# Performance work log

Measured on AMD Instinct MI355X. Metric: run time of the kernel, lower is better.

## Reference

```python
import jax, jax.numpy as jnp
import numpy as np

T = 4          # num edge types
D = 256        # embedding_size == hidden_size
N = 100_000    # nodes
E_EDGES = 320_000
VOCAB = 10_000


def setup_inputs() -> dict:
    key = jax.random.key(0)
    ks = jax.random.split(key, 12)
    s = 0.02
    input_ids = jax.random.randint(ks[0], (1, N), 0, VOCAB)
    etype = jax.random.randint(ks[1], (1, E_EDGES), 1, T + 1)  # types 1..T
    src = jax.random.randint(ks[2], (1, E_EDGES), 0, N)
    tgt = jax.random.randint(ks[3], (1, E_EDGES), 0, N)
    typed_edges = jnp.stack([etype[0], src[0], tgt[0]], axis=0)[None]  # [1,3,E]
    embed_table = jax.random.normal(ks[4], (VOCAB, D)) * s
    # 6 inner layers (3 per concat block x 2 blocks): 256 -> 256
    edge_W_inner = jax.random.normal(ks[5], (6, T, D, 2 * D)) * s
    ln_s_inner = jnp.ones((6, D)); ln_b_inner = jnp.zeros((6, D))
    dense_W_inner = jax.random.normal(ks[6], (6, D, D)) * s
    dense_b_inner = jnp.zeros((6, D))
    # 2 output layers on concat [state, hidden]: hidden_size 512 -> 256
    edge_W_out = jax.random.normal(ks[7], (2, T, 2 * D, 4 * D)) * s
    ln_s_out = jnp.ones((2, 2 * D)); ln_b_out = jnp.zeros((2, 2 * D))
    dense_W_out = jax.random.normal(ks[8], (2, D, 2 * D)) * s
    dense_b_out = jnp.zeros((2, D))
    return {
        "input_ids": input_ids, "typed_edges": typed_edges,
        "embed_table": embed_table,
        "edge_W_inner": edge_W_inner, "ln_s_inner": ln_s_inner, "ln_b_inner": ln_b_inner,
        "dense_W_inner": dense_W_inner, "dense_b_inner": dense_b_inner,
        "edge_W_out": edge_W_out, "ln_s_out": ln_s_out, "ln_b_out": ln_b_out,
        "dense_W_out": dense_W_out, "dense_b_out": dense_b_out,
    }


def layer_norm(x, s, b, eps=1e-5):
    mu = jnp.mean(x, axis=-1, keepdims=True)
    var = jnp.mean((x - mu) ** 2, axis=-1, keepdims=True)
    return (x - mu) * jax.lax.rsqrt(var + eps) * s + b


def message_passing(state, etype, src, tgt, edge_W):
    # state [N,d]; edge_W [T, d, 2d]. Gather endpoints, per-type linear, scatter-add to targets.
    es = jnp.concatenate([state[src], state[tgt]], axis=1)  # [E, 2d]
    msgs = jnp.zeros((es.shape[0], edge_W.shape[1]), state.dtype)
    for t in range(edge_W.shape[0]):  # small fixed number of edge types
        msgs = msgs + jnp.where((etype == t + 1)[:, None], es @ edge_W[t].T, 0.0)
    return jax.ops.segment_sum(msgs, tgt, num_segments=state.shape[0])


def gnn_layer(state, etype, src, tgt, eW, ls, lb, dW, db):
    m = message_passing(state, etype, src, tgt, eW)
    h = layer_norm(jax.nn.gelu(m, approximate=False), ls, lb)
    return jnp.tanh(h @ dW.T + db)


def concat_block(state, etype, src, tgt, eWi, lsi, lbi, dWi, dbi, eWo, lso, lbo, dWo, dbo):
    x = state
    for i in range(3):
        x = gnn_layer(x, etype, src, tgt, eWi[i], lsi[i], lbi[i], dWi[i], dbi[i])
    res = jnp.concatenate([state, x], axis=1)  # [N, 2d] residual concat
    return gnn_layer(res, etype, src, tgt, eWo, lso, lbo, dWo, dbo)


def reference(input_ids, typed_edges, embed_table, edge_W_inner, ln_s_inner, ln_b_inner,
              dense_W_inner, dense_b_inner, edge_W_out, ln_s_out, ln_b_out,
              dense_W_out, dense_b_out):
    ids = input_ids[0]
    te = typed_edges[0]
    etype, src, tgt = te[0], te[1], te[2]
    x = embed_table[ids]  # [N, D]
    for b in range(2):
        sl = slice(3 * b, 3 * b + 3)
        x = concat_block(x, etype, src, tgt,
                         edge_W_inner[sl], ln_s_inner[sl], ln_b_inner[sl],
                         dense_W_inner[sl], dense_b_inner[sl],
                         edge_W_out[b], ln_s_out[b], ln_b_out[b],
                         dense_W_out[b], dense_b_out[b])
    return x
```

## Files before the change

kernel.cpp:

```cpp
#include <hip/hip_runtime.h>
#include <cstdio>

#define N_NODES 100000
#define NPAD    100096
#define NTILES  782
#define NE      320000
#define NCH     196
#define WCO_OFF 3145728L
#define OUT_ELEMS (N_NODES * 256)

typedef unsigned short ushort_t;
typedef unsigned short u16x4 __attribute__((ext_vector_type(4)));
typedef unsigned short u16x8 __attribute__((ext_vector_type(8)));
typedef _Float16       f16;
typedef _Float16       f16x8 __attribute__((ext_vector_type(8)));
typedef float          f32x4 __attribute__((ext_vector_type(4)));
typedef float          f32x4v __attribute__((ext_vector_type(4)));

__device__ __forceinline__ float bf2f(ushort_t u) {
    return __uint_as_float(((unsigned)u) << 16);
}
__device__ __forceinline__ ushort_t f2bf(float f) {
    unsigned u = __float_as_uint(f);
    u += 0x7FFFu + ((u >> 16) & 1u);
    return (ushort_t)(u >> 16);
}
__device__ __forceinline__ ushort_t f2h(float f) {
    f16 h = (f16)f;
    return __builtin_bit_cast(ushort_t, h);
}
__device__ __forceinline__ float h2f(ushort_t u) {
    return (float)__builtin_bit_cast(f16, u);
}

__global__ __launch_bounds__(256) void detect_k(const unsigned* __restrict__ w0, int* __restrict__ flag) {
    __shared__ int lds[256];
    int t = threadIdx.x;
    int cnt = 0;
    for (int i = t; i < 2048; i += 256) {
        unsigned e = (w0[i] >> 7) & 0xFFu;
        cnt += (e >= 96u && e <= 140u) ? 1 : 0;
    }
    lds[t] = cnt; __syncthreads();
    for (int s = 128; s > 0; s >>= 1) {
        if (t < s) lds[t] += lds[t + s];
        __syncthreads();
    }
    if (t == 0) *flag = (lds[0] < 1024) ? 1 : 0;
}

__device__ __forceinline__ ushort_t load_in(const void* p, long i, bool isf32) {
    return isf32 ? f2h(((const float*)p)[i]) : f2h(bf2f(((const ushort_t*)p)[i]));
}

struct CvtArgs {
    const void* src[8];
    ushort_t*   dst[8];
    int         n[8];
};

__global__ __launch_bounds__(256) void cvt_k(CvtArgs a, const int* __restrict__ flag) {
    int ti = blockIdx.y;
    int n = a.n[ti];
    const void* s = a.src[ti];
    ushort_t* d = a.dst[ti];
    bool isf32 = (*flag != 0);
    for (int i = blockIdx.x * 256 + threadIdx.x; i < n; i += gridDim.x * 256)
        d[i] = load_in(s, i, isf32);
}

__global__ __launch_bounds__(256) void pack_w(const void* __restrict__ eWi,
                                              const void* __restrict__ eWo,
                                              ushort_t* __restrict__ WC,
                                              const int* __restrict__ flag) {
    long idx = (long)blockIdx.x * 256 + threadIdx.x;
    bool isf32 = (*flag != 0);
    const long ELI = 6L * 4 * 256 * 512;
    const long ELO = 2L * 4 * 512 * 1024;
    if (idx < ELI) {
        int j = idx & 511;
        int o = (idx >> 9) & 255;
        int t = (idx >> 17) & 3;
        long l = idx >> 19;
        int q = o >> 6, oo = o & 63;
        int k = j & 255;
        int n = ((j < 256) ? 0 : 256) + t * 64 + oo;
        WC[l * 524288 + (long)q * 131072 + (long)n * 256 + k] = load_in(eWi, idx, isf32);
    } else if (idx < ELI + ELO) {
        long i2 = idx - ELI;
        int j = i2 & 1023;
        int o = (i2 >> 10) & 511;
        int t = (i2 >> 19) & 3;
        long b = i2 >> 21;
        int p = t >> 1, ts = t & 1;
        WC[WCO_OFF + (b * 2 + p) * 1048576L + (long)o * 2048 + ts * 1024 + j] = load_in(eWo, i2, isf32);
    }
}

__global__ __launch_bounds__(256) void embed_k(const int* __restrict__ ids,
                                               const void* __restrict__ tab,
                                               ushort_t* __restrict__ S,
                                               const int* __restrict__ flag) {
    int row = blockIdx.x * 4 + (threadIdx.x >> 6);
    int l = threadIdx.x & 63;
    if (row >= N_NODES) return;
    int id = ids[row];
    u16x4 v;
    if (*flag) {
        f32x4v fv = *(const f32x4v*)((const float*)tab + (size_t)id * 256 + l * 4);
        #pragma unroll
        for (int i = 0; i < 4; i++) v[i] = f2h(fv[i]);
    } else {
        u16x4 bv = *(const u16x4*)((const ushort_t*)tab + (size_t)id * 256 + l * 4);
        #pragma unroll
        for (int i = 0; i < 4; i++) v[i] = f2h(bf2f(bv[i]));
    }
    *(u16x4*)(S + (size_t)row * 256 + l * 4) = v;
}

__global__ __launch_bounds__(256) void emit_k(const ushort_t* __restrict__ Bst, void* __restrict__ out,
                                              const int* __restrict__ flag) {
    long i = (long)blockIdx.x * 256 + threadIdx.x;
    if (i >= OUT_ELEMS) return;
    float v = h2f(Bst[i]);
    if (*flag) ((float*)out)[i] = v;
    else       ((ushort_t*)out)[i] = f2bf(v);
}

__global__ __launch_bounds__(256) void count_k(const int* __restrict__ tgt, int* __restrict__ counts) {
    int e = blockIdx.x * 256 + threadIdx.x;
    if (e < NE) atomicAdd(&counts[tgt[e]], 1);
}

__global__ __launch_bounds__(256) void scan1_k(const int* __restrict__ counts,
                                               int* __restrict__ incl, int* __restrict__ chsums) {
    __shared__ int lds[256];
    int c = blockIdx.x, t = threadIdx.x;
    int i0 = c * 512 + 2 * t;
    int a = (i0 < N_NODES) ? counts[i0] : 0;
    int b = (i0 + 1 < N_NODES) ? counts[i0 + 1] : 0;
    int ps = a + b;
    lds[t] = ps; __syncthreads();
    int x = ps;
    for (int off = 1; off < 256; off <<= 1) {
        int y = (t >= off) ? lds[t - off] : 0;
        __syncthreads();
        x += y; lds[t] = x;
        __syncthreads();
    }
    int excl = x - ps;
    if (i0 < N_NODES) incl[i0] = excl + a;
    if (i0 + 1 < N_NODES) incl[i0 + 1] = excl + a + b;
    if (t == 255) chsums[c] = x;
}

__global__ __launch_bounds__(256) void scan2_k(const int* __restrict__ chsums, int* __restrict__ chunkoff) {
    __shared__ int lds[256];
    int t = threadIdx.x;
    int v = (t < NCH) ? chsums[t] : 0;
    lds[t] = v; __syncthreads();
    int x = v;
    for (int off = 1; off < 256; off <<= 1) {
        int y = (t >= off) ? lds[t - off] : 0;
        __syncthreads();
        x += y; lds[t] = x;
        __syncthreads();
    }
    if (t <= NCH) chunkoff[t] = x - v;
}

__global__ __launch_bounds__(256) void scan3_k(const int* __restrict__ counts, const int* __restrict__ incl,
                                               const int* __restrict__ chunkoff,
                                               int* __restrict__ offsets, int* __restrict__ cursor) {
    int c = blockIdx.x, t = threadIdx.x;
    int base = chunkoff[c];
    #pragma unroll
    for (int k = 0; k < 2; k++) {
        int i = c * 512 + 2 * t + k;
        if (i < N_NODES) {
            int off = base + incl[i] - counts[i];
            offsets[i] = off;
            cursor[i] = off;
        }
    }
    if (c == 0 && t == 0) offsets[N_NODES] = chunkoff[NCH];
}

__global__ __launch_bounds__(256) void fill_k(const int* __restrict__ et, const int* __restrict__ src,
                                              const int* __restrict__ tgt,
                                              int* __restrict__ cursor, int* __restrict__ sorted) {
    int e = blockIdx.x * 256 + threadIdx.x;
    if (e < NE) {
        int pos = atomicAdd(&cursor[tgt[e]], 1);
        sorted[pos] = ((et[e] - 1) << 28) | src[e];
    }
}

template<int DIN>
__device__ __forceinline__ void load_row(const ushort_t* __restrict__ X0, const ushort_t* __restrict__ X1,
                                         size_t r, int l, float* out) {
    if constexpr (DIN == 256) {
        u16x4 rv = *(const u16x4*)(X0 + r * 256 + l * 4);
        #pragma unroll
        for (int i = 0; i < 4; i++) out[i] = h2f(rv[i]);
    } else {
        const ushort_t* bp = (l < 32) ? (X0 + r * 256 + (size_t)l * 8)
                                      : (X1 + r * 256 + (size_t)(l - 32) * 8);
        u16x8 rv = *(const u16x8*)bp;
        #pragma unroll
        for (int i = 0; i < 8; i++) out[i] = h2f(rv[i]);
    }
}

template<int DIN>
__device__ __forceinline__ void store_blk(ushort_t* __restrict__ G, size_t base, int l,
                                          const float* A, int D, const float* xv) {
    if constexpr (DIN == 256) {
        u16x4 o1, o2;
        #pragma unroll
        for (int i = 0; i < 4; i++) { o1[i] = f2h(A[i]); o2[i] = f2h((float)D * xv[i]); }
        *(u16x4*)(G + base + l * 4) = o1;
        *(u16x4*)(G + base + DIN + l * 4) = o2;
    } else {
        u16x8 o1, o2;
        #pragma unroll
        for (int i = 0; i < 8; i++) { o1[i] = f2h(A[i]); o2[i] = f2h((float)D * xv[i]); }
        *(u16x8*)(G + base + l * 8) = o1;
        *(u16x8*)(G + base + DIN + l * 8) = o2;
    }
}

template<int DIN, int NT>
__global__ __launch_bounds__(256) void build_g(const ushort_t* __restrict__ X0, const ushort_t* __restrict__ X1,
                                               const int* __restrict__ offsets, const int* __restrict__ sorted,
                                               ushort_t* __restrict__ G, int t0, int vbase) {
    constexpr int VPL = DIN / 64;
    int vl = blockIdx.x * 4 + (threadIdx.x >> 6);
    int l = threadIdx.x & 63;
    int v = vbase + vl;
    float a0[VPL] = {}, a1[VPL] = {}, a2[VPL] = {}, a3[VPL] = {};
    int d0 = 0, d1 = 0, d2 = 0, d3 = 0;
    float xv[VPL];
    #pragma unroll
    for (int i = 0; i < VPL; i++) xv[i] = 0.f;
    if (v < N_NODES) {
        int beg = offsets[v], end = offsets[v + 1];
        for (int e = beg; e < end; ++e) {
            int pk = sorted[e];
            int t = (pk >> 28) - t0;
            if ((unsigned)t >= (unsigned)NT) continue;
            int s = pk & 0x0FFFFFFF;
            float rvf[VPL];
            load_row<DIN>(X0, X1, (size_t)s, l, rvf);
            if (t == 0) { d0++;
                #pragma unroll
                for (int i = 0; i < VPL; i++) a0[i] += rvf[i]; }
            else if (t == 1) { d1++;
                #pragma unroll
                for (int i = 0; i < VPL; i++) a1[i] += rvf[i]; }
            else if (NT > 2 && t == 2) { d2++;
                #pragma unroll
                for (int i = 0; i < VPL; i++) a2[i] += rvf[i]; }
            else { d3++;
                #pragma unroll
                for (int i = 0; i < VPL; i++) a3[i] += rvf[i]; }
        }
        load_row<DIN>(X0, X1, (size_t)v, l, xv);
    }
    size_t rowb = (size_t)vl * 2048;
    store_blk<DIN>(G, rowb + 0 * 2 * DIN, l, a0, d0, xv);
    store_blk<DIN>(G, rowb + 1 * 2 * DIN, l, a1, d1, xv);
    if constexpr (NT > 2) {
        store_blk<DIN>(G, rowb + 2 * 2 * DIN, l, a2, d2, xv);
        store_blk<DIN>(G, rowb + 3 * 2 * DIN, l, a3, d3, xv);
    }
}

template<int EPI>
__global__ __launch_bounds__(256) void gemm_bt(const ushort_t* __restrict__ A,
                                               const ushort_t* __restrict__ B,
                                               int K, int ldc,
                                               float* __restrict__ Cf, ushort_t* __restrict__ Cb,
                                               const ushort_t* __restrict__ bias, int storeM) {
    __shared__ __align__(16) ushort_t As[128 * 64];
    __shared__ __align__(16) ushort_t Bs[128 * 64];
    const int tid = threadIdx.x;
    const int w = tid >> 6, l = tid & 63;
    const int wr = w >> 1, wc = w & 1;
    const long m0 = (long)blockIdx.y * 128, n0 = (long)blockIdx.x * 128;
    const int lr = l >> 3;
    const int lc = (l & 7) * 8;
    f32x4 acc[4][4];
    #pragma unroll
    for (int s = 0; s < 4; s++)
        #pragma unroll
        for (int n = 0; n < 4; n++) acc[s][n] = (f32x4){0.f, 0.f, 0.f, 0.f};

    for (int k0 = 0; k0 < K; k0 += 64) {
        #pragma unroll
        for (int q = 0; q < 4; q++) {
            int row = w * 32 + q * 8 + lr;
            const ushort_t* g = A + (m0 + row) * (long)K + k0 + lc;
            __builtin_amdgcn_global_load_lds(
                (__attribute__((address_space(1))) unsigned int*)(g),
                (__attribute__((address_space(3))) unsigned int*)(&As[row * 64 + lc]), 16, 0, 0);
        }
        #pragma unroll
        for (int q = 0; q < 4; q++) {
            int row = w * 32 + q * 8 + lr;
            const ushort_t* g = B + (n0 + row) * (long)K + k0 + lc;
            __builtin_amdgcn_global_load_lds(
                (__attribute__((address_space(1))) unsigned int*)(g),
                (__attribute__((address_space(3))) unsigned int*)(&Bs[row * 64 + lc]), 16, 0, 0);
        }
        __syncthreads();
        #pragma unroll
        for (int kk = 0; kk < 2; kk++) {
            f16x8 af[4], bfr[4];
            #pragma unroll
            for (int s = 0; s < 4; s++)
                af[s] = *(const f16x8*)&As[(wr * 64 + s * 16 + (l & 15)) * 64 + kk * 32 + (l >> 4) * 8];
            #pragma unroll
            for (int n = 0; n < 4; n++)
                bfr[n] = *(const f16x8*)&Bs[(wc * 64 + n * 16 + (l & 15)) * 64 + kk * 32 + (l >> 4) * 8];
            #pragma unroll
            for (int s = 0; s < 4; s++)
                #pragma unroll
                for (int n = 0; n < 4; n++)
                    acc[s][n] = __builtin_amdgcn_mfma_f32_16x16x32_f16(af[s], bfr[n], acc[s][n], 0, 0, 0);
        }
        __syncthreads();
    }
    const long rb = m0 + wr * 64 + ((l >> 4) << 2);
    const long cb = n0 + wc * 64 + (l & 15);
    #pragma unroll
    for (int s = 0; s < 4; s++) {
        #pragma unroll
        for (int n = 0; n < 4; n++) {
            long c = cb + n * 16;
            #pragma unroll
            for (int j = 0; j < 4; j++) {
                long r = rb + s * 16 + j;
                float val = acc[s][n][j];
                if constexpr (EPI == 0) {
                    Cf[r * ldc + c] = val;
                } else if constexpr (EPI == 1) {
                    Cf[r * ldc + c] += val;
                } else if constexpr (EPI == 2) {
                    if (r < storeM) {
                        float t = tanhf(val + h2f(bias[c]));
                        Cb[r * ldc + c] = f2h(t);
                    }
                } else {
                    Cb[r * ldc + c] = f2h(val);
                }
            }
        }
    }
}

__global__ __launch_bounds__(256) void agg_q(const ushort_t* __restrict__ Z,
                                             const int* __restrict__ offsets,
                                             const int* __restrict__ sorted,
                                             ushort_t* __restrict__ Magg, int q) {
    int v = blockIdx.x * 4 + (threadIdx.x >> 6);
    int l = threadIdx.x & 63;
    if (v >= NPAD) return;
    ushort_t* mp = Magg + (size_t)v * 256 + (q << 6) + l;
    if (v >= N_NODES) { *mp = 0; return; }
    float acc = 0.f;
    int d0 = 0, d1 = 0, d2 = 0, d3 = 0;
    int beg = offsets[v], end = offsets[v + 1];
    for (int e = beg; e < end; ++e) {
        int pk = sorted[e];
        int t = pk >> 28;
        int s = pk & 0x0FFFFFFF;
        acc += h2f(Z[(size_t)s * 512 + (t << 6) + l]);
        d0 += (t == 0); d1 += (t == 1); d2 += (t == 2); d3 += (t == 3);
    }
    const ushort_t* zs = Z + (size_t)v * 512 + 256 + l;
    if (d0) acc += (float)d0 * h2f(zs[0]);
    if (d1) acc += (float)d1 * h2f(zs[64]);
    if (d2) acc += (float)d2 * h2f(zs[128]);
    if (d3) acc += (float)d3 * h2f(zs[192]);
    *mp = f2h(acc);
}

__global__ __launch_bounds__(256) void gelu_ln16_k(const ushort_t* __restrict__ M,
                                                   const ushort_t* __restrict__ ls,
                                                   const ushort_t* __restrict__ lb,
                                                   ushort_t* __restrict__ H) {
    int row = blockIdx.x * 4 + (threadIdx.x >> 6);
    int l = threadIdx.x & 63;
    u16x4 mv = *(const u16x4*)(M + (size_t)row * 256 + l * 4);
    float g[4];
    float s = 0.f, q = 0.f;
    #pragma unroll
    for (int i = 0; i < 4; i++) {
        float x = h2f(mv[i]);
        float gg = 0.5f * x * (1.f + erff(x * 0.70710678118654752f));
        g[i] = gg; s += gg; q += gg * gg;
    }
    #pragma unroll
    for (int m = 1; m < 64; m <<= 1) {
        s += __shfl_xor(s, m, 64);
        q += __shfl_xor(q, m, 64);
    }
    float mean = s * (1.f / 256.f);
    float var = q * (1.f / 256.f) - mean * mean;
    var = fmaxf(var, 0.f);
    float rs = rsqrtf(var + 1e-5f);
    int col = l << 2;
    u16x4 o;
    #pragma unroll
    for (int i = 0; i < 4; i++)
        o[i] = f2h((g[i] - mean) * rs * h2f(ls[col + i]) + h2f(lb[col + i]));
    *(u16x4*)(H + (size_t)row * 256 + col) = o;
}

template<int DOUT>
__global__ __launch_bounds__(256) void gelu_ln_k(const float* __restrict__ Mf,
                                                 const ushort_t* __restrict__ ls,
                                                 const ushort_t* __restrict__ lb,
                                                 ushort_t* __restrict__ H) {
    constexpr int VPL = DOUT / 64;
    int row = blockIdx.x * 4 + (threadIdx.x >> 6);
    int l = threadIdx.x & 63;
    const float* p = Mf + (size_t)row * DOUT + l * VPL;
    float g[VPL];
    float s = 0.f, q = 0.f;
    #pragma unroll
    for (int i = 0; i < VPL; i++) {
        float x = p[i];
        float gg = 0.5f * x * (1.f + erff(x * 0.70710678118654752f));
        g[i] = gg; s += gg; q += gg * gg;
    }
    #pragma unroll
    for (int m = 1; m < 64; m <<= 1) {
        s += __shfl_xor(s, m, 64);
        q += __shfl_xor(q, m, 64);
    }
    float mean = s * (1.f / DOUT);
    float var = q * (1.f / DOUT) - mean * mean;
    var = fmaxf(var, 0.f);
    float rs = rsqrtf(var + 1e-5f);
    ushort_t* hp = H + (size_t)row * DOUT + l * VPL;
    #pragma unroll
    for (int i = 0; i < VPL; i++) {
        int col = l * VPL + i;
        hp[i] = f2h((g[i] - mean) * rs * h2f(ls[col]) + h2f(lb[col]));
    }
}

extern "C" void kernel_launch(void* const* d_in, const int* in_sizes, int n_in,
                              void* d_out, int out_size, void* d_ws, size_t ws_size,
                              hipStream_t stream) {
    const int* ids = (const int*)d_in[0];
    const int* te = (const int*)d_in[1];
    const int* et = te;
    const int* esrc = te + NE;
    const int* etgt = te + 2 * NE;
    const void* tab = d_in[2];
    const void* eWi = d_in[3];
    const void* lsi = d_in[4];
    const void* lbi = d_in[5];
    const void* dWi = d_in[6];
    const void* dbi = d_in[7];
    const void* eWo = d_in[8];
    const void* lso = d_in[9];
    const void* lbo = d_in[10];
    const void* dWo = d_in[11];
    const void* dbo = d_in[12];

    char* w = (char*)d_ws;
    auto alloc = [&](size_t bytes) -> char* {
        char* p = w; w += (bytes + 255) & ~(size_t)255; return p;
    };
    ushort_t* A    = (ushort_t*)alloc((size_t)NPAD * 256 * 2);
    ushort_t* Bst  = (ushort_t*)alloc((size_t)NPAD * 256 * 2);
    ushort_t* WC   = (ushort_t*)alloc(7340032UL * 2);
    ushort_t* lsiC = (ushort_t*)alloc(1536 * 2);
    ushort_t* lbiC = (ushort_t*)alloc(1536 * 2);
    ushort_t* dbiC = (ushort_t*)alloc(1536 * 2);
    ushort_t* lsoC = (ushort_t*)alloc(1024 * 2);
    ushort_t* lboC = (ushort_t*)alloc(1024 * 2);
    ushort_t* dboC = (ushort_t*)alloc(512 * 2);
    ushort_t* dWiC = (ushort_t*)alloc(393216UL * 2);
    ushort_t* dWoC = (ushort_t*)alloc(262144UL * 2);
    int* flag      = (int*)alloc(256);
    int* counts    = (int*)alloc((size_t)N_NODES * 4);
    int* incl      = (int*)alloc((size_t)N_NODES * 4);
    int* chsums    = (int*)alloc(1024);
    int* chunkoff  = (int*)alloc(1024);
    int* offsets   = (int*)alloc((size_t)(N_NODES + 8) * 4);
    int* cursor    = (int*)alloc((size_t)N_NODES * 4);
    int* sorted    = (int*)alloc((size_t)NE * 4);
    ushort_t* Magg = (ushort_t*)alloc((size_t)NPAD * 256 * 2);
    ushort_t* R;
    if ((size_t)out_size >= (size_t)NPAD * 256 * 2) R = (ushort_t*)d_out;
    else R = (ushort_t*)alloc((size_t)NPAD * 256 * 2);
    size_t fixed = (size_t)(w - (char*)d_ws);

    const size_t ZQ_BYTES = (size_t)NPAD * 512 * 2;
    const size_t PER_TILE = 128UL * 2048 * 2 + 128UL * 512 * 4 + 128UL * 512 * 2;
    size_t bigsz = (ws_size > fixed) ? (ws_size - fixed) : 0;
    long tiles_chunk = (long)(bigsz / PER_TILE);
    if (tiles_chunk > NTILES) tiles_chunk = NTILES;
    if (bigsz < ZQ_BYTES || tiles_chunk < 1) {
        fprintf(stderr, "kernel_launch: ws too small (%zu bytes, fixed %zu, big %zu) -- no-op\n",
                ws_size, fixed, bigsz);
        return;
    }
    char* big = w;
    ushort_t* Zq   = (ushort_t*)big;
    ushort_t* Hin  = (ushort_t*)big;
    ushort_t* G    = (ushort_t*)big;
    float*    Mf   = (float*)(big + (size_t)tiles_chunk * 524288);
    ushort_t* Hc   = (ushort_t*)(big + (size_t)tiles_chunk * (524288 + 262144));

    detect_k<<<1, 256, 0, stream>>>((const unsigned*)tab, flag);
    CvtArgs ca;
    ca.src[0] = lsi;  ca.dst[0] = lsiC; ca.n[0] = 1536;
    ca.src[1] = lbi;  ca.dst[1] = lbiC; ca.n[1] = 1536;
    ca.src[2] = dbi;  ca.dst[2] = dbiC; ca.n[2] = 1536;
    ca.src[3] = lso;  ca.dst[3] = lsoC; ca.n[3] = 1024;
    ca.src[4] = lbo;  ca.dst[4] = lboC; ca.n[4] = 1024;
    ca.src[5] = dbo;  ca.dst[5] = dboC; ca.n[5] = 512;
    ca.src[6] = dWi;  ca.dst[6] = dWiC; ca.n[6] = 393216;
    ca.src[7] = dWo;  ca.dst[7] = dWoC; ca.n[7] = 262144;
    cvt_k<<<dim3(1536, 8), 256, 0, stream>>>(ca, flag);
    hipMemsetAsync(counts, 0, (size_t)N_NODES * 4, stream);
    hipMemsetAsync(A   + (size_t)N_NODES * 256, 0, (size_t)(NPAD - N_NODES) * 256 * 2, stream);
    hipMemsetAsync(Bst + (size_t)N_NODES * 256, 0, (size_t)(NPAD - N_NODES) * 256 * 2, stream);
    hipMemsetAsync(R   + (size_t)N_NODES * 256, 0, (size_t)(NPAD - N_NODES) * 256 * 2, stream);
    pack_w<<<28672, 256, 0, stream>>>(eWi, eWo, WC, flag);
    embed_k<<<N_NODES / 4, 256, 0, stream>>>(ids, tab, A, flag);
    count_k<<<(NE + 255) / 256, 256, 0, stream>>>(etgt, counts);
    scan1_k<<<NCH, 256, 0, stream>>>(counts, incl, chsums);
    scan2_k<<<1, 256, 0, stream>>>(chsums, chunkoff);
    scan3_k<<<NCH, 256, 0, stream>>>(counts, incl, chunkoff, offsets, cursor);
    fill_k<<<(NE + 255) / 256, 256, 0, stream>>>(et, esrc, etgt, cursor, sorted);

    auto inner_layer = [&](const ushort_t* Xin, ushort_t* Xout, int lay) {
        for (int q = 0; q < 4; q++) {
            gemm_bt<3><<<dim3(4, NTILES), 256, 0, stream>>>(
                Xin, WC + (long)lay * 524288 + (long)q * 131072, 256, 512,
                nullptr, Zq, nullptr, 0);
            agg_q<<<NPAD / 4, 256, 0, stream>>>(Zq, offsets, sorted, Magg, q);
        }
        gelu_ln16_k<<<NPAD / 4, 256, 0, stream>>>(Magg, lsiC + lay * 256, lbiC + lay * 256, Hin);
        gemm_bt<2><<<dim3(2, NTILES), 256, 0, stream>>>(Hin, dWiC + (long)lay * 65536, 256, 256,
                                                        nullptr, Xout, dbiC + lay * 256, N_NODES);
    };

    auto out_layer = [&](const ushort_t* X0, const ushort_t* X1, int b, ushort_t* dest) {
        for (long t0t = 0; t0t < NTILES; t0t += tiles_chunk) {
            long tc = NTILES - t0t; if (tc > tiles_chunk) tc = tiles_chunk;
            long rows = tc * 128, mb = t0t * 128;
            build_g<512, 2><<<rows / 4, 256, 0, stream>>>(X0, X1, offsets, sorted, G, 0, (int)mb);
            gemm_bt<0><<<dim3(4, tc), 256, 0, stream>>>(G, WC + WCO_OFF + (long)(b * 2 + 0) * 1048576,
                                                        2048, 512, Mf, nullptr, nullptr, 0);
            build_g<512, 2><<<rows / 4, 256, 0, stream>>>(X0, X1, offsets, sorted, G, 2, (int)mb);
            gemm_bt<1><<<dim3(4, tc), 256, 0, stream>>>(G, WC + WCO_OFF + (long)(b * 2 + 1) * 1048576,
                                                        2048, 512, Mf, nullptr, nullptr, 0);
            gelu_ln_k<512><<<rows / 4, 256, 0, stream>>>(Mf, lsoC + b * 512, lboC + b * 512, Hc);
            long sM = (long)N_NODES - mb; if (sM > rows) sM = rows; if (sM < 0) sM = 0;
            gemm_bt<2><<<dim3(2, tc), 256, 0, stream>>>(Hc, dWoC + (long)b * 131072, 512, 256,
                                                        nullptr, dest + mb * 256, dboC + b * 256, (int)sM);
        }
    };

    inner_layer(A, Bst, 0);
    inner_layer(Bst, R, 1);
    inner_layer(R, Bst, 2);
    out_layer(A, Bst, 0, R);
    inner_layer(R, A, 3);
    inner_layer(A, Bst, 4);
    inner_layer(Bst, A, 5);
    out_layer(R, A, 1, Bst);

    emit_k<<<(OUT_ELEMS + 255) / 256, 256, 0, stream>>>(Bst, d_out, flag);
}
```

Measured before the change: 6.816 ms.

## Restructure output layers to transform-then-aggregate like inner layers

The output-layer path used to build a per-node aggregated feature matrix G of width 2048 and then run a K=2048 GEMM into fp32. It now follows the inner-layer scheme: a per-node GEMM over the concatenated input (K=512) in 8 column chunks, with edge aggregation applied to the transformed outputs, then a shared GELU+LN kernel. This removes the heavy gather-heavy build_g and the large-K GEMMs, cutting FLOPs. The cost is more kernel launches (8 GEMM+agg pairs) and fp16 intermediate storage where fp32 was used before.

```diff
diff --git a/kernel.cpp b/kernel.cpp
--- a/kernel.cpp
+++ b/kernel.cpp
@@ -92,8 +92,10 @@
         int o = (i2 >> 10) & 511;
         int t = (i2 >> 19) & 3;
         long b = i2 >> 21;
-        int p = t >> 1, ts = t & 1;
-        WC[WCO_OFF + (b * 2 + p) * 1048576L + (long)o * 2048 + ts * 1024 + j] = load_in(eWo, i2, isf32);
+        int c = o >> 6, oo = o & 63;
+        int k = j & 511;
+        int n = ((j < 512) ? 0 : 256) + t * 64 + oo;
+        WC[WCO_OFF + b * 2097152L + (long)c * 262144 + (long)n * 512 + k] = load_in(eWo, i2, isf32);
     }
 }
 
@@ -196,91 +198,11 @@
     }
 }
 
-template<int DIN>
-__device__ __forceinline__ void load_row(const ushort_t* __restrict__ X0, const ushort_t* __restrict__ X1,
-                                         size_t r, int l, float* out) {
-    if constexpr (DIN == 256) {
-        u16x4 rv = *(const u16x4*)(X0 + r * 256 + l * 4);
-        #pragma unroll
-        for (int i = 0; i < 4; i++) out[i] = h2f(rv[i]);
-    } else {
-        const ushort_t* bp = (l < 32) ? (X0 + r * 256 + (size_t)l * 8)
-                                      : (X1 + r * 256 + (size_t)(l - 32) * 8);
-        u16x8 rv = *(const u16x8*)bp;
-        #pragma unroll
-        for (int i = 0; i < 8; i++) out[i] = h2f(rv[i]);
-    }
-}
-
-template<int DIN>
-__device__ __forceinline__ void store_blk(ushort_t* __restrict__ G, size_t base, int l,
-                                          const float* A, int D, const float* xv) {
-    if constexpr (DIN == 256) {
-        u16x4 o1, o2;
-        #pragma unroll
-        for (int i = 0; i < 4; i++) { o1[i] = f2h(A[i]); o2[i] = f2h((float)D * xv[i]); }
-        *(u16x4*)(G + base + l * 4) = o1;
-        *(u16x4*)(G + base + DIN + l * 4) = o2;
-    } else {
-        u16x8 o1, o2;
-        #pragma unroll
-        for (int i = 0; i < 8; i++) { o1[i] = f2h(A[i]); o2[i] = f2h((float)D * xv[i]); }
-        *(u16x8*)(G + base + l * 8) = o1;
-        *(u16x8*)(G + base + DIN + l * 8) = o2;
-    }
-}
-
-template<int DIN, int NT>
-__global__ __launch_bounds__(256) void build_g(const ushort_t* __restrict__ X0, const ushort_t* __restrict__ X1,
-                                               const int* __restrict__ offsets, const int* __restrict__ sorted,
-                                               ushort_t* __restrict__ G, int t0, int vbase) {
-    constexpr int VPL = DIN / 64;
-    int vl = blockIdx.x * 4 + (threadIdx.x >> 6);
-    int l = threadIdx.x & 63;
-    int v = vbase + vl;
-    float a0[VPL] = {}, a1[VPL] = {}, a2[VPL] = {}, a3[VPL] = {};
-    int d0 = 0, d1 = 0, d2 = 0, d3 = 0;
-    float xv[VPL];
-    #pragma unroll
-    for (int i = 0; i < VPL; i++) xv[i] = 0.f;
-    if (v < N_NODES) {
-        int beg = offsets[v], end = offsets[v + 1];
-        for (int e = beg; e < end; ++e) {
-            int pk = sorted[e];
-            int t = (pk >> 28) - t0;
-            if ((unsigned)t >= (unsigned)NT) continue;
-            int s = pk & 0x0FFFFFFF;
-            float rvf[VPL];
-            load_row<DIN>(X0, X1, (size_t)s, l, rvf);
-            if (t == 0) { d0++;
-                #pragma unroll
-                for (int i = 0; i < VPL; i++) a0[i] += rvf[i]; }
-            else if (t == 1) { d1++;
-                #pragma unroll
-                for (int i = 0; i < VPL; i++) a1[i] += rvf[i]; }
-            else if (NT > 2 && t == 2) { d2++;
-                #pragma unroll
-                for (int i = 0; i < VPL; i++) a2[i] += rvf[i]; }
-            else { d3++;
-                #pragma unroll
-                for (int i = 0; i < VPL; i++) a3[i] += rvf[i]; }
-        }
-        load_row<DIN>(X0, X1, (size_t)v, l, xv);
-    }
-    size_t rowb = (size_t)vl * 2048;
-    store_blk<DIN>(G, rowb + 0 * 2 * DIN, l, a0, d0, xv);
-    store_blk<DIN>(G, rowb + 1 * 2 * DIN, l, a1, d1, xv);
-    if constexpr (NT > 2) {
-        store_blk<DIN>(G, rowb + 2 * 2 * DIN, l, a2, d2, xv);
-        store_blk<DIN>(G, rowb + 3 * 2 * DIN, l, a3, d3, xv);
-    }
-}
-
 template<int EPI>
 __global__ __launch_bounds__(256) void gemm_bt(const ushort_t* __restrict__ A,
                                                const ushort_t* __restrict__ B,
                                                int K, int ldc,
-                                               float* __restrict__ Cf, ushort_t* __restrict__ Cb,
+                                               ushort_t* __restrict__ Cb,
                                                const ushort_t* __restrict__ bias, int storeM) {
     __shared__ __align__(16) ushort_t As[128 * 64];
     __shared__ __align__(16) ushort_t Bs[128 * 64];
@@ -342,11 +264,7 @@
             for (int j = 0; j < 4; j++) {
                 long r = rb + s * 16 + j;
                 float val = acc[s][n][j];
-                if constexpr (EPI == 0) {
-                    Cf[r * ldc + c] = val;
-                } else if constexpr (EPI == 1) {
-                    Cf[r * ldc + c] += val;
-                } else if constexpr (EPI == 2) {
+                if constexpr (EPI == 2) {
                     if (r < storeM) {
                         float t = tanhf(val + h2f(bias[c]));
                         Cb[r * ldc + c] = f2h(t);
@@ -359,14 +277,86 @@
     }
 }
 
+__global__ __launch_bounds__(256) void gemm_bt2(const ushort_t* __restrict__ A0,
+                                                const ushort_t* __restrict__ A1,
+                                                const ushort_t* __restrict__ B,
+                                                int ldc,
+                                                ushort_t* __restrict__ Cb) {
+    __shared__ __align__(16) ushort_t As[128 * 64];
+    __shared__ __align__(16) ushort_t Bs[128 * 64];
+    const int tid = threadIdx.x;
+    const int w = tid >> 6, l = tid & 63;
+    const int wr = w >> 1, wc = w & 1;
+    const long m0 = (long)blockIdx.y * 128, n0 = (long)blockIdx.x * 128;
+    const int lr = l >> 3;
+    const int lc = (l & 7) * 8;
+    f32x4 acc[4][4];
+    #pragma unroll
+    for (int s = 0; s < 4; s++)
+        #pragma unroll
+        for (int n = 0; n < 4; n++) acc[s][n] = (f32x4){0.f, 0.f, 0.f, 0.f};
+
+    for (int k0 = 0; k0 < 512; k0 += 64) {
+        const ushort_t* Ab = (k0 < 256) ? A0 : A1;
+        const int kq = k0 & 255;
+        #pragma unroll
+        for (int q = 0; q < 4; q++) {
+            int row = w * 32 + q * 8 + lr;
+            const ushort_t* g = Ab + (m0 + row) * 256L + kq + lc;
+            __builtin_amdgcn_global_load_lds(
+                (__attribute__((address_space(1))) unsigned int*)(g),
+                (__attribute__((address_space(3))) unsigned int*)(&As[row * 64 + lc]), 16, 0, 0);
+        }
+        #pragma unroll
+        for (int q = 0; q < 4; q++) {
+            int row = w * 32 + q * 8 + lr;
+            const ushort_t* g = B + (n0 + row) * 512L + k0 + lc;
+            __builtin_amdgcn_global_load_lds(
+                (__attribute__((address_space(1))) unsigned int*)(g),
+                (__attribute__((address_space(3))) unsigned int*)(&Bs[row * 64 + lc]), 16, 0, 0);
+        }
+        __syncthreads();
+        #pragma unroll
+        for (int kk = 0; kk < 2; kk++) {
+            f16x8 af[4], bfr[4];
+            #pragma unroll
+            for (int s = 0; s < 4; s++)
+                af[s] = *(const f16x8*)&As[(wr * 64 + s * 16 + (l & 15)) * 64 + kk * 32 + (l >> 4) * 8];
+            #pragma unroll
+            for (int n = 0; n < 4; n++)
+                bfr[n] = *(const f16x8*)&Bs[(wc * 64 + n * 16 + (l & 15)) * 64 + kk * 32 + (l >> 4) * 8];
+            #pragma unroll
+            for (int s = 0; s < 4; s++)
+                #pragma unroll
+                for (int n = 0; n < 4; n++)
+                    acc[s][n] = __builtin_amdgcn_mfma_f32_16x16x32_f16(af[s], bfr[n], acc[s][n], 0, 0, 0);
+        }
+        __syncthreads();
+    }
+    const long rb = m0 + wr * 64 + ((l >> 4) << 2);
+    const long cb = n0 + wc * 64 + (l & 15);
+    #pragma unroll
+    for (int s = 0; s < 4; s++) {
+        #pragma unroll
+        for (int n = 0; n < 4; n++) {
+            long c = cb + n * 16;
+            #pragma unroll
+            for (int j = 0; j < 4; j++) {
+                long r = rb + s * 16 + j;
+                Cb[r * ldc + c] = f2h(acc[s][n][j]);
+            }
+        }
+    }
+}
+
 __global__ __launch_bounds__(256) void agg_q(const ushort_t* __restrict__ Z,
                                              const int* __restrict__ offsets,
                                              const int* __restrict__ sorted,
-                                             ushort_t* __restrict__ Magg, int q) {
+                                             ushort_t* __restrict__ M, int mld, int q) {
     int v = blockIdx.x * 4 + (threadIdx.x >> 6);
     int l = threadIdx.x & 63;
     if (v >= NPAD) return;
-    ushort_t* mp = Magg + (size_t)v * 256 + (q << 6) + l;
+    ushort_t* mp = M + (size_t)v * mld + (q << 6) + l;
     if (v >= N_NODES) { *mp = 0; return; }
     float acc = 0.f;
     int d0 = 0, d1 = 0, d2 = 0, d3 = 0;
@@ -386,52 +376,23 @@
     *mp = f2h(acc);
 }
 
+template<int DOUT>
 __global__ __launch_bounds__(256) void gelu_ln16_k(const ushort_t* __restrict__ M,
                                                    const ushort_t* __restrict__ ls,
                                                    const ushort_t* __restrict__ lb,
                                                    ushort_t* __restrict__ H) {
-    int row = blockIdx.x * 4 + (threadIdx.x >> 6);
-    int l = threadIdx.x & 63;
-    u16x4 mv = *(const u16x4*)(M + (size_t)row * 256 + l * 4);
-    float g[4];
-    float s = 0.f, q = 0.f;
-    #pragma unroll
-    for (int i = 0; i < 4; i++) {
-        float x = h2f(mv[i]);
-        float gg = 0.5f * x * (1.f + erff(x * 0.70710678118654752f));
-        g[i] = gg; s += gg; q += gg * gg;
-    }
-    #pragma unroll
-    for (int m = 1; m < 64; m <<= 1) {
-        s += __shfl_xor(s, m, 64);
-        q += __shfl_xor(q, m, 64);
-    }
-    float mean = s * (1.f / 256.f);
-    float var = q * (1.f / 256.f) - mean * mean;
-    var = fmaxf(var, 0.f);
-    float rs = rsqrtf(var + 1e-5f);
-    int col = l << 2;
-    u16x4 o;
-    #pragma unroll
-    for (int i = 0; i < 4; i++)
-        o[i] = f2h((g[i] - mean) * rs * h2f(ls[col + i]) + h2f(lb[col + i]));
-    *(u16x4*)(H + (size_t)row * 256 + col) = o;
-}
-
-template<int DOUT>
-__global__ __launch_bounds__(256) void gelu_ln_k(const float* __restrict__ Mf,
-                                                 const ushort_t* __restrict__ ls,
-                                                 const ushort_t* __restrict__ lb,
-                                                 ushort_t* __restrict__ H) {
     constexpr int VPL = DOUT / 64;
     int row = blockIdx.x * 4 + (threadIdx.x >> 6);
     int l = threadIdx.x & 63;
-    const float* p = Mf + (size_t)row * DOUT + l * VPL;
+    const ushort_t* mp = M + (size_t)row * DOUT + l * VPL;
+    u16x4 mv[VPL / 4];
+    #pragma unroll
+    for (int c = 0; c < VPL / 4; c++) mv[c] = *(const u16x4*)(mp + c * 4);
     float g[VPL];
     float s = 0.f, q = 0.f;
     #pragma unroll
     for (int i = 0; i < VPL; i++) {
-        float x = p[i];
+        float x = h2f(mv[i >> 2][i & 3]);
         float gg = 0.5f * x * (1.f + erff(x * 0.70710678118654752f));
         g[i] = gg; s += gg; q += gg * gg;
     }
@@ -444,12 +405,11 @@
     float var = q * (1.f / DOUT) - mean * mean;
     var = fmaxf(var, 0.f);
     float rs = rsqrtf(var + 1e-5f);
-    ushort_t* hp = H + (size_t)row * DOUT + l * VPL;
-    #pragma unroll
-    for (int i = 0; i < VPL; i++) {
-        int col = l * VPL + i;
-        hp[i] = f2h((g[i] - mean) * rs * h2f(ls[col]) + h2f(lb[col]));
-    }
+    int col = l * VPL;
+    ushort_t* hp = H + (size_t)row * DOUT + col;
+    #pragma unroll
+    for (int i = 0; i < VPL; i++)
+        hp[i] = f2h((g[i] - mean) * rs * h2f(ls[col + i]) + h2f(lb[col + i]));
 }
 
 extern "C" void kernel_launch(void* const* d_in, const int* in_sizes, int n_in,
@@ -495,28 +455,21 @@
     int* offsets   = (int*)alloc((size_t)(N_NODES + 8) * 4);
     int* cursor    = (int*)alloc((size_t)N_NODES * 4);
     int* sorted    = (int*)alloc((size_t)NE * 4);
-    ushort_t* Magg = (ushort_t*)alloc((size_t)NPAD * 256 * 2);
+    ushort_t* Magg = (ushort_t*)alloc((size_t)NPAD * 512 * 2);
     ushort_t* R;
     if ((size_t)out_size >= (size_t)NPAD * 256 * 2) R = (ushort_t*)d_out;
     else R = (ushort_t*)alloc((size_t)NPAD * 256 * 2);
     size_t fixed = (size_t)(w - (char*)d_ws);
 
     const size_t ZQ_BYTES = (size_t)NPAD * 512 * 2;
-    const size_t PER_TILE = 128UL * 2048 * 2 + 128UL * 512 * 4 + 128UL * 512 * 2;
     size_t bigsz = (ws_size > fixed) ? (ws_size - fixed) : 0;
-    long tiles_chunk = (long)(bigsz / PER_TILE);
-    if (tiles_chunk > NTILES) tiles_chunk = NTILES;
-    if (bigsz < ZQ_BYTES || tiles_chunk < 1) {
+    if (bigsz < ZQ_BYTES) {
         fprintf(stderr, "kernel_launch: ws too small (%zu bytes, fixed %zu, big %zu) -- no-op\n",
                 ws_size, fixed, bigsz);
         return;
     }
-    char* big = w;
-    ushort_t* Zq   = (ushort_t*)big;
-    ushort_t* Hin  = (ushort_t*)big;
-    ushort_t* G    = (ushort_t*)big;
-    float*    Mf   = (float*)(big + (size_t)tiles_chunk * 524288);
-    ushort_t* Hc   = (ushort_t*)(big + (size_t)tiles_chunk * (524288 + 262144));
+    ushort_t* Zq = (ushort_t*)w;
+    ushort_t* H  = (ushort_t*)w;
 
     detect_k<<<1, 256, 0, stream>>>((const unsigned*)tab, flag);
     CvtArgs ca;
@@ -544,30 +497,23 @@
     auto inner_layer = [&](const ushort_t* Xin, ushort_t* Xout, int lay) {
         for (int q = 0; q < 4; q++) {
             gemm_bt<3><<<dim3(4, NTILES), 256, 0, stream>>>(
-                Xin, WC + (long)lay * 524288 + (long)q * 131072, 256, 512,
-                nullptr, Zq, nullptr, 0);
-            agg_q<<<NPAD / 4, 256, 0, stream>>>(Zq, offsets, sorted, Magg, q);
-        }
-        gelu_ln16_k<<<NPAD / 4, 256, 0, stream>>>(Magg, lsiC + lay * 256, lbiC + lay * 256, Hin);
-        gemm_bt<2><<<dim3(2, NTILES), 256, 0, stream>>>(Hin, dWiC + (long)lay * 65536, 256, 256,
-                                                        nullptr, Xout, dbiC + lay * 256, N_NODES);
+                Xin, WC + (long)lay * 524288 + (long)q * 131072, 256, 512, Zq, nullptr, 0);
+            agg_q<<<NPAD / 4, 256, 0, stream>>>(Zq, offsets, sorted, Magg, 256, q);
+        }
+        gelu_ln16_k<256><<<NPAD / 4, 256, 0, stream>>>(Magg, lsiC + lay * 256, lbiC + lay * 256, H);
+        gemm_bt<2><<<dim3(2, NTILES), 256, 0, stream>>>(H, dWiC + (long)lay * 65536, 256, 256,
+                                                        Xout, dbiC + lay * 256, N_NODES);
     };
 
     auto out_layer = [&](const ushort_t* X0, const ushort_t* X1, int b, ushort_t* dest) {
-        for (long t0t = 0; t0t < NTILES; t0t += tiles_chunk) {
-            long tc = NTILES - t0t; if (tc > tiles_chunk) tc = tiles_chunk;
-            long rows = tc * 128, mb = t0t * 128;
-            build_g<512, 2><<<rows / 4, 256, 0, stream>>>(X0, X1, offsets, sorted, G, 0, (int)mb);
-            gemm_bt<0><<<dim3(4, tc), 256, 0, stream>>>(G, WC + WCO_OFF + (long)(b * 2 + 0) * 1048576,
-                                                        2048, 512, Mf, nullptr, nullptr, 0);
-            build_g<512, 2><<<rows / 4, 256, 0, stream>>>(X0, X1, offsets, sorted, G, 2, (int)mb);
-            gemm_bt<1><<<dim3(4, tc), 256, 0, stream>>>(G, WC + WCO_OFF + (long)(b * 2 + 1) * 1048576,
-                                                        2048, 512, Mf, nullptr, nullptr, 0);
-            gelu_ln_k<512><<<rows / 4, 256, 0, stream>>>(Mf, lsoC + b * 512, lboC + b * 512, Hc);
-            long sM = (long)N_NODES - mb; if (sM > rows) sM = rows; if (sM < 0) sM = 0;
-            gemm_bt<2><<<dim3(2, tc), 256, 0, stream>>>(Hc, dWoC + (long)b * 131072, 512, 256,
-                                                        nullptr, dest + mb * 256, dboC + b * 256, (int)sM);
-        }
+        for (int c = 0; c < 8; c++) {
+            gemm_bt2<<<dim3(4, NTILES), 256, 0, stream>>>(
+                X0, X1, WC + WCO_OFF + (long)b * 2097152 + (long)c * 262144, 512, Zq);
+            agg_q<<<NPAD / 4, 256, 0, stream>>>(Zq, offsets, sorted, Magg, 512, c);
+        }
+        gelu_ln16_k<512><<<NPAD / 4, 256, 0, stream>>>(Magg, lsoC + b * 512, lboC + b * 512, H);
+        gemm_bt<2><<<dim3(2, NTILES), 256, 0, stream>>>(H, dWoC + (long)b * 131072, 512, 256,
+                                                        dest, dboC + b * 256, N_NODES);
     };
 
     inner_layer(A, Bst, 0);
```

Measured after the change: 6.489 ms. -4.8%, faster.
